# Optimization experiments

Hardware: AMD Instinct MI355X
Metric: run time of the kernel (lower is better)

Reference implementation:

```python
import jax, jax.numpy as jnp
import numpy as np
import math

HIDDEN = 2048
NUM_HEADS = 16
HEAD_DIM = HIDDEN // NUM_HEADS  # 128
B, T = 2, 2048
MAX_POS = 4096
ROPE_BASE = 10000.0


def _rope_cache(dim, max_pos, base):
    inv_freq = 1.0 / (base ** (jnp.arange(0, dim, 2, dtype=jnp.float32) / dim))
    t = jnp.arange(max_pos, dtype=jnp.float32)
    freqs = jnp.einsum('i,j->ij', t, inv_freq)        # [max_pos, dim/2]
    emb = jnp.concatenate([freqs, freqs], axis=-1)     # [max_pos, dim]
    return jnp.cos(emb), jnp.sin(emb)


def setup_inputs() -> dict:
    key = jax.random.key(0)
    ks = jax.random.split(key, 5)
    hidden_states = jax.random.normal(ks[0], (B, T, HIDDEN), dtype=jnp.float32)
    # additive causal mask, large negative (not -inf) for numerical safety
    causal = jnp.triu(jnp.full((T, T), -1e9, dtype=jnp.float32), k=1)
    attention_mask = causal[None, None, :, :]          # [1,1,T,T]
    position_ids = jnp.arange(T, dtype=jnp.int64)
    s = 1.0 / math.sqrt(HIDDEN)
    Wq = jax.random.normal(ks[1], (HIDDEN, HIDDEN), dtype=jnp.float32) * s
    Wk = jax.random.normal(ks[2], (HIDDEN, HIDDEN), dtype=jnp.float32) * s
    Wv = jax.random.normal(ks[3], (HIDDEN, HIDDEN), dtype=jnp.float32) * s
    Wo = jax.random.normal(ks[4], (HIDDEN, HIDDEN), dtype=jnp.float32) * s
    cos_cached, sin_cached = _rope_cache(HEAD_DIM, MAX_POS, ROPE_BASE)
    return {
        'hidden_states': hidden_states,
        'attention_mask': attention_mask,
        'position_ids': position_ids,
        'Wq': Wq, 'Wk': Wk, 'Wv': Wv, 'Wo': Wo,
        'cos_cached': cos_cached, 'sin_cached': sin_cached,
    }


def _apply_rope(x, cos, sin):
    # x: [B, T, nh, hd]; cos/sin: [T, 1, hd] (broadcast over heads)
    x1 = x[..., 0::2]
    x2 = x[..., 1::2]
    x_rot = jnp.stack([-x2, x1], axis=-1).reshape(x.shape)  # interleaved rotate
    return x * cos + x_rot * sin


def reference(hidden_states, attention_mask, position_ids, Wq, Wk, Wv, Wo,
              cos_cached, sin_cached):
    Bs, Ts, H = hidden_states.shape
    nh, hd = NUM_HEADS, HEAD_DIM
    q = (hidden_states @ Wq.T).reshape(Bs, Ts, nh, hd)
    k = (hidden_states @ Wk.T).reshape(Bs, Ts, nh, hd)
    v = (hidden_states @ Wv.T).reshape(Bs, Ts, nh, hd)
    cos = cos_cached[position_ids][:, None, :]  # [T,1,hd]
    sin = sin_cached[position_ids][:, None, :]
    q = _apply_rope(q, cos, sin)
    k = _apply_rope(k, cos, sin)
    # [B, nh, T, hd]
    q = q.transpose(0, 2, 1, 3)
    k = k.transpose(0, 2, 1, 3)
    v = v.transpose(0, 2, 1, 3)
    scores = jnp.einsum('bhqd,bhkd->bhqk', q, k) / math.sqrt(hd)
    scores = scores + attention_mask
    attn = jax.nn.softmax(scores, axis=-1)
    out = jnp.einsum('bhqk,bhkd->bhqd', attn, v)
    out = out.transpose(0, 2, 1, 3).reshape(Bs, Ts, H)
    return out @ Wo.T
```

## Files before the change

kernel.cpp:

```cpp
#include <hip/hip_runtime.h>
#include <cstdint>


typedef __bf16 v8bf __attribute__((ext_vector_type(8)));
typedef float  v4f  __attribute__((ext_vector_type(4)));
typedef float  f32x16 __attribute__((ext_vector_type(16)));

__device__ __forceinline__ uint16_t f2bf(float f) {
  union { float f; uint32_t u; } v; v.f = f;
  uint32_t u = v.u;
  return (uint16_t)((u + 0x7FFFu + ((u >> 16) & 1u)) >> 16);
}

__device__ __forceinline__ uint32_t cvtpk(float lo, float hi) {
  uint32_t w;
  asm("v_cvt_pk_bf16_f32 %0, %1, %2" : "=v"(w) : "v"(lo), "v"(hi));
  return w;
}

__device__ __forceinline__ void gload16(const void* g, void* l) {
  __builtin_amdgcn_global_load_lds(
      (const __attribute__((address_space(1))) void*)g,
      (__attribute__((address_space(3))) void*)l, 16, 0, 0);
}

__global__ void cvt_all_kernel(const float* __restrict__ s0, uint16_t* d0,
                               const float* __restrict__ s1, uint16_t* d1,
                               const float* __restrict__ s2, uint16_t* d2,
                               const float* __restrict__ s3, uint16_t* d3,
                               const float* __restrict__ s4, uint16_t* d4) {
  const float* src; uint16_t* dst; int n4;
  switch (blockIdx.y) {
    case 0: src = s0; dst = d0; n4 = 2097152; break;
    case 1: src = s1; dst = d1; n4 = 1048576; break;
    case 2: src = s2; dst = d2; n4 = 1048576; break;
    case 3: src = s3; dst = d3; n4 = 1048576; break;
    default: src = s4; dst = d4; n4 = 1048576; break;
  }
  int i = blockIdx.x * blockDim.x + threadIdx.x;
  int stride = gridDim.x * blockDim.x;
  for (; i < n4; i += stride) {
    float4 v = reinterpret_cast<const float4*>(src)[i];
    ushort4 o;
    o.x = f2bf(v.x); o.y = f2bf(v.y); o.z = f2bf(v.z); o.w = f2bf(v.w);
    reinterpret_cast<ushort4*>(dst)[i] = o;
  }
}

__device__ __forceinline__ void gemm128_mainloop(
    const uint16_t* __restrict__ A, const uint16_t* __restrict__ Bt,
    int m0, int n0, uint16_t* As, uint16_t* Bs, v4f acc[4][4]) {
  const int tid  = threadIdx.x;
  const int lane = tid & 63;
  const int w    = tid >> 6;
  const int wr   = w >> 1, wc = w & 1;
  const int lrow = lane & 15;
  const int lk8  = (lane >> 4) * 8;

  for (int k0 = 0; k0 < 2048; k0 += 64) {
#pragma unroll
    for (int i = 0; i < 4; ++i) {
      int chunk = i * 256 + tid;
      int row = chunk >> 3, seg = chunk & 7;
      gload16(A + (size_t)(m0 + row) * 2048 + k0 + seg * 8, As + chunk * 8);
    }
#pragma unroll
    for (int i = 0; i < 4; ++i) {
      int chunk = i * 256 + tid;
      int row = chunk >> 3, seg = chunk & 7;
      gload16(Bt + (size_t)(n0 + row) * 2048 + k0 + seg * 8, Bs + chunk * 8);
    }
    __syncthreads();
#pragma unroll
    for (int ks = 0; ks < 2; ++ks) {
      v8bf af[4], bfv[4];
#pragma unroll
      for (int mf = 0; mf < 4; ++mf)
        af[mf] = *reinterpret_cast<const v8bf*>(
            As + (wr * 64 + mf * 16 + lrow) * 64 + ks * 32 + lk8);
#pragma unroll
      for (int nf = 0; nf < 4; ++nf)
        bfv[nf] = *reinterpret_cast<const v8bf*>(
            Bs + (wc * 64 + nf * 16 + lrow) * 64 + ks * 32 + lk8);
#pragma unroll
      for (int mf = 0; mf < 4; ++mf)
#pragma unroll
        for (int nf = 0; nf < 4; ++nf)
          acc[mf][nf] = __builtin_amdgcn_mfma_f32_16x16x32_bf16(
              af[mf], bfv[nf], acc[mf][nf], 0, 0, 0);
    }
    __syncthreads();
  }
}

__global__ __launch_bounds__(256) void qkv_gemm_kernel(
    const uint16_t* __restrict__ Xbf,
    const uint16_t* __restrict__ Wqb, const uint16_t* __restrict__ Wkb,
    const uint16_t* __restrict__ Wvb,
    const float* __restrict__ cosc, const float* __restrict__ sinc,
    uint16_t* __restrict__ Qh, uint16_t* __restrict__ Kh,
    uint16_t* __restrict__ Vt) {
  __shared__ uint16_t As[128 * 64];
  __shared__ uint16_t Bs[128 * 64];
  const int id  = (blockIdx.z * 32 + blockIdx.y) * 16 + blockIdx.x;
  const int swz = (id & 7) * 192 + (id >> 3);
  const int which = swz >> 9;
  const int m0 = ((swz >> 4) & 31) * 128, n0 = (swz & 15) * 128;
  const uint16_t* Wb = (which == 0) ? Wqb : (which == 1) ? Wkb : Wvb;

  v4f acc[4][4];
#pragma unroll
  for (int i = 0; i < 4; ++i)
#pragma unroll
    for (int j = 0; j < 4; ++j) acc[i][j] = (v4f)0.0f;

  gemm128_mainloop(Xbf, Wb, m0, n0, As, Bs, acc);

  const int lane = threadIdx.x & 63;
  const int w = threadIdx.x >> 6, wr = w >> 1, wc = w & 1;
  const int lrow = lane & 15, lhi = lane >> 4;
  const int b = m0 >> 11;

  if (which < 2) {
    uint16_t* dst = (which == 0) ? Qh : Kh;
#pragma unroll
    for (int mf = 0; mf < 4; ++mf) {
#pragma unroll
      for (int nf = 0; nf < 4; ++nf) {
        const int n = n0 + wc * 64 + nf * 16 + lrow;
        const int head = n >> 7, d = n & 127;
#pragma unroll
        for (int r = 0; r < 4; ++r) {
          const int m = m0 + wr * 64 + mf * 16 + lhi * 4 + r;
          const int t = m & 2047;
          float v = acc[mf][nf][r];
          float p = __shfl_xor(v, 1);
          float rot = (n & 1) ? p : -p;
          float cf = cosc[t * 128 + d], sf = sinc[t * 128 + d];
          dst[((size_t)(b * 16 + head) * 2048 + t) * 128 + d] =
              f2bf(v * cf + rot * sf);
        }
      }
    }
  } else {
#pragma unroll
    for (int mf = 0; mf < 4; ++mf) {
#pragma unroll
      for (int nf = 0; nf < 4; ++nf) {
        const int n = n0 + wc * 64 + nf * 16 + lrow;
        const int head = n >> 7, d = n & 127;
        const int m = m0 + wr * 64 + mf * 16 + lhi * 4;
        const int t = m & 2047;
        ushort4 o;
        o.x = f2bf(acc[mf][nf][0]); o.y = f2bf(acc[mf][nf][1]);
        o.z = f2bf(acc[mf][nf][2]); o.w = f2bf(acc[mf][nf][3]);
        *reinterpret_cast<ushort4*>(
            &Vt[((size_t)(b * 16 + head) * 128 + d) * 2048 + t]) = o;
      }
    }
  }
}

__global__ __launch_bounds__(256, 2) void attn_kernel(
    const uint16_t* __restrict__ Qh, const uint16_t* __restrict__ Kh,
    const uint16_t* __restrict__ Vt, uint16_t* __restrict__ Ob) {
  __shared__ uint16_t Ks[2 * 64 * 128];
  __shared__ uint16_t Vs[2 * 128 * 64];

  const int id = blockIdx.x;
  const int qt = (id < 256) ? (15 - (id >> 5)) : ((id - 256) >> 5);
  const int bh = id & 31;
  const int tid = threadIdx.x, lane = tid & 63, w = tid >> 6;
  const int l31 = lane & 31, hi = lane >> 5;
  const size_t base = (size_t)bh * 2048 * 128;
  const int q0 = qt * 128 + w * 32;
  const int qr = q0 + l31;

  v8bf qf[8];
#pragma unroll
  for (int ks = 0; ks < 8; ++ks)
    qf[ks] = *reinterpret_cast<const v8bf*>(
        Qh + base + (size_t)qr * 128 + ks * 16 + hi * 8);

  f32x16 acc[4];
#pragma unroll
  for (int d = 0; d < 4; ++d) acc[d] = (f32x16)0.0f;
  float m = -1e30f, l = 0.0f;

  auto stage = [&](int buf, int kt) {
    uint16_t* Kd = Ks + buf * 8192;
    uint16_t* Vd = Vs + buf * 8192;
#pragma unroll
    for (int i = 0; i < 4; ++i) {
      int c = i * 256 + tid;
      int row = c >> 4, seg = c & 15;
      int sseg = seg ^ (row & 7);
      gload16(Kh + base + (size_t)(kt * 64 + row) * 128 + sseg * 8,
              Kd + c * 8);
    }
#pragma unroll
    for (int i = 0; i < 4; ++i) {
      int c = i * 256 + tid;
      int row = c >> 3, seg = c & 7;
      int sseg = seg ^ (row & 7);
      gload16(Vt + base + (size_t)row * 2048 + kt * 64 + sseg * 8,
              Vd + c * 8);
    }
  };

  const float sc = 0.08838834764831845f;
  const int nkt = 2 * (qt + 1);
  stage(0, 0);
  for (int kt = 0; kt < nkt; ++kt) {
    const int cur = kt & 1;
    __syncthreads();
    if (kt + 1 < nkt) stage(cur ^ 1, kt + 1);
    const uint16_t* Kc = Ks + cur * 8192;
    const uint16_t* Vc = Vs + cur * 8192;

    if (kt * 64 <= q0 + 31) {
      f32x16 s[2];
      s[0] = (f32x16)0.0f; s[1] = (f32x16)0.0f;
#pragma unroll
      for (int kb = 0; kb < 2; ++kb) {
        const int row = kb * 32 + l31;
        const int swz = row & 7;
#pragma unroll
        for (int ks = 0; ks < 8; ++ks) {
          const int seg = (ks * 2 + hi) ^ swz;
          v8bf kf = *reinterpret_cast<const v8bf*>(Kc + row * 128 + seg * 8);
          s[kb] = __builtin_amdgcn_mfma_f32_32x32x16_bf16(kf, qf[ks], s[kb],
                                                          0, 0, 0);
        }
      }
      if (kt * 64 + 63 > q0) {
#pragma unroll
        for (int kb = 0; kb < 2; ++kb)
#pragma unroll
          for (int q = 0; q < 4; ++q)
#pragma unroll
            for (int r = 0; r < 4; ++r) {
              const int kc = kt * 64 + kb * 32 + q * 8 + hi * 4 + r;
              float v = s[kb][q * 4 + r] * sc;
              s[kb][q * 4 + r] = (kc > qr) ? -1e30f : v;
            }
      } else {
#pragma unroll
        for (int kb = 0; kb < 2; ++kb)
#pragma unroll
          for (int g = 0; g < 16; ++g) s[kb][g] *= sc;
      }
      float t8[8];
#pragma unroll
      for (int g = 0; g < 8; ++g)
        t8[g] = fmaxf(fmaxf(s[0][g], s[0][g + 8]),
                      fmaxf(s[1][g], s[1][g + 8]));
      float mx = fmaxf(fmaxf(fmaxf(t8[0], t8[1]), fmaxf(t8[2], t8[3])),
                       fmaxf(fmaxf(t8[4], t8[5]), fmaxf(t8[6], t8[7])));
      mx = fmaxf(mx, __shfl_xor(mx, 32));
      if (!__all(mx - m <= 8.0f)) {
        const float mnew = fmaxf(m, mx);
        const float so = __expf(m - mnew);
        m = mnew;
        l *= so;
#pragma unroll
        for (int d = 0; d < 4; ++d)
#pragma unroll
          for (int g = 0; g < 16; ++g) acc[d][g] *= so;
      }
      float rs = 0.0f;
#pragma unroll
      for (int kb = 0; kb < 2; ++kb)
#pragma unroll
        for (int g = 0; g < 16; ++g) {
          const float pv = __expf(s[kb][g] - m);
          s[kb][g] = pv;
          rs += pv;
        }
      rs += __shfl_xor(rs, 32);
      l += rs;
      union BW { uint32_t w[4]; v8bf v; };
      BW pb[4];
#pragma unroll
      for (int kb = 0; kb < 2; ++kb)
#pragma unroll
        for (int sl = 0; sl < 2; ++sl) {
          uint32_t a0 = cvtpk(s[kb][8 * sl + 0], s[kb][8 * sl + 1]);
          uint32_t a1 = cvtpk(s[kb][8 * sl + 2], s[kb][8 * sl + 3]);
          uint32_t b0 = cvtpk(s[kb][8 * sl + 4], s[kb][8 * sl + 5]);
          uint32_t b1 = cvtpk(s[kb][8 * sl + 6], s[kb][8 * sl + 7]);
          asm("v_permlane32_swap_b32 %0, %1" : "+v"(a0), "+v"(b0));
          asm("v_permlane32_swap_b32 %0, %1" : "+v"(a1), "+v"(b1));
          BW& f = pb[kb * 2 + sl];
          f.w[0] = a0; f.w[1] = a1; f.w[2] = b0; f.w[3] = b1;
        }
#pragma unroll
      for (int d = 0; d < 4; ++d) {
        const int row = d * 32 + l31;
        const int swz = row & 7;
#pragma unroll
        for (int sl4 = 0; sl4 < 4; ++sl4) {
          const int seg = (sl4 * 2 + hi) ^ swz;
          v8bf va = *reinterpret_cast<const v8bf*>(Vc + row * 64 + seg * 8);
          acc[d] = __builtin_amdgcn_mfma_f32_32x32x16_bf16(va, pb[sl4].v,
                                                           acc[d], 0, 0, 0);
        }
      }
    }
  }

  const int b = bh >> 4, head = bh & 15;
  const float inv = 1.0f / l;
#pragma unroll
  for (int d = 0; d < 4; ++d)
#pragma unroll
    for (int q = 0; q < 4; ++q)
#pragma unroll
      for (int rp = 0; rp < 2; ++rp) {
        const int dd = d * 32 + q * 8 + hi * 4 + rp * 2;
        const uint32_t lo16 = f2bf(acc[d][q * 4 + rp * 2] * inv);
        const uint32_t hi16 = f2bf(acc[d][q * 4 + rp * 2 + 1] * inv);
        *reinterpret_cast<uint32_t*>(
            &Ob[((size_t)(b * 2048 + qr)) * 2048 + head * 128 + dd]) =
            lo16 | (hi16 << 16);
      }
}

__global__ __launch_bounds__(256) void out_gemm_kernel(
    const uint16_t* __restrict__ Abf, const uint16_t* __restrict__ Wob,
    float* __restrict__ out) {
  __shared__ uint16_t As[128 * 64];
  __shared__ uint16_t Bs[128 * 64];
  const int id  = blockIdx.y * 16 + blockIdx.x;
  const int swz = (id & 7) * 64 + (id >> 3);
  const int m0 = (swz >> 4) * 128, n0 = (swz & 15) * 128;
  v4f acc[4][4];
#pragma unroll
  for (int i = 0; i < 4; ++i)
#pragma unroll
    for (int j = 0; j < 4; ++j) acc[i][j] = (v4f)0.0f;

  gemm128_mainloop(Abf, Wob, m0, n0, As, Bs, acc);

  const int lane = threadIdx.x & 63;
  const int w = threadIdx.x >> 6, wr = w >> 1, wc = w & 1;
  const int lrow = lane & 15, lhi = lane >> 4;
#pragma unroll
  for (int mf = 0; mf < 4; ++mf)
#pragma unroll
    for (int nf = 0; nf < 4; ++nf) {
      const int n = n0 + wc * 64 + nf * 16 + lrow;
#pragma unroll
      for (int r = 0; r < 4; ++r) {
        const int m = m0 + wr * 64 + mf * 16 + lhi * 4 + r;
        out[(size_t)m * 2048 + n] = acc[mf][nf][r];
      }
    }
}

extern "C" void kernel_launch(void* const* d_in, const int* in_sizes, int n_in,
                              void* d_out, int out_size, void* d_ws,
                              size_t ws_size, hipStream_t stream) {
  const float* hidden = (const float*)d_in[0];
  const float* Wq = (const float*)d_in[3];
  const float* Wk = (const float*)d_in[4];
  const float* Wv = (const float*)d_in[5];
  const float* Wo = (const float*)d_in[6];
  const float* cosc = (const float*)d_in[7];
  const float* sinc = (const float*)d_in[8];
  float* out = (float*)d_out;

  uint16_t* Wqb = (uint16_t*)d_ws;
  uint16_t* Wkb = Wqb + 4194304;
  uint16_t* Wvb = Wkb + 4194304;
  uint16_t* Wvb2 = Wvb;
  uint16_t* Wob = Wvb + 4194304;
  uint16_t* Xbf = Wob + 4194304;
  uint16_t* Qh  = Xbf + 8388608;
  uint16_t* Kh  = Qh + 8388608;
  uint16_t* Vt  = Kh + 8388608;
  uint16_t* Ob  = Xbf;
  (void)Wvb2;

  cvt_all_kernel<<<dim3(512, 5), 256, 0, stream>>>(
      hidden, Xbf, Wq, Wqb, Wk, Wkb, Wv, Wvb, Wo, Wob);

  qkv_gemm_kernel<<<dim3(16, 32, 3), 256, 0, stream>>>(
      Xbf, Wqb, Wkb, Wvb, cosc, sinc, Qh, Kh, Vt);

  attn_kernel<<<dim3(512), 256, 0, stream>>>(Qh, Kh, Vt, Ob);

  out_gemm_kernel<<<dim3(16, 32), 256, 0, stream>>>(Ob, Wob, out);
}
```

Before: 435.8 us.

## Double-buffer GEMM LDS tiles with XOR swizzle to overlap loads and MFMA

Rewrites the shared GEMM mainloop so the global-to-LDS load of the next K tile is issued into a second buffer while the current tile is consumed, with one barrier per iteration instead of two. LDS reads use an XOR swizzle of the 16-byte segment by row to avoid bank conflicts. Both GEMM kernels get doubled LDS (64KB) and launch_bounds with a minimum of 2 blocks, which trades LDS capacity and register budget for the overlap.

```diff
diff --git a/kernel.cpp b/kernel.cpp
--- a/kernel.cpp
+++ b/kernel.cpp
@@ -55,33 +55,48 @@
   const int w    = tid >> 6;
   const int wr   = w >> 1, wc = w & 1;
   const int lrow = lane & 15;
-  const int lk8  = (lane >> 4) * 8;
-
-  for (int k0 = 0; k0 < 2048; k0 += 64) {
+  const int lhi  = lane >> 4;
+
+  auto stage = [&](int buf, int k0) {
+    uint16_t* Ad = As + buf * 8192;
+    uint16_t* Bd = Bs + buf * 8192;
 #pragma unroll
     for (int i = 0; i < 4; ++i) {
-      int chunk = i * 256 + tid;
-      int row = chunk >> 3, seg = chunk & 7;
-      gload16(A + (size_t)(m0 + row) * 2048 + k0 + seg * 8, As + chunk * 8);
+      int c = i * 256 + tid;
+      int row = c >> 3, seg = c & 7;
+      int sseg = seg ^ (row & 7);
+      gload16(A + (size_t)(m0 + row) * 2048 + k0 + sseg * 8, Ad + c * 8);
     }
 #pragma unroll
     for (int i = 0; i < 4; ++i) {
-      int chunk = i * 256 + tid;
-      int row = chunk >> 3, seg = chunk & 7;
-      gload16(Bt + (size_t)(n0 + row) * 2048 + k0 + seg * 8, Bs + chunk * 8);
-    }
+      int c = i * 256 + tid;
+      int row = c >> 3, seg = c & 7;
+      int sseg = seg ^ (row & 7);
+      gload16(Bt + (size_t)(n0 + row) * 2048 + k0 + sseg * 8, Bd + c * 8);
+    }
+  };
+
+  stage(0, 0);
+  for (int t = 0; t < 32; ++t) {
     __syncthreads();
+    if (t + 1 < 32) stage((t + 1) & 1, (t + 1) * 64);
+    const uint16_t* Ac = As + (t & 1) * 8192;
+    const uint16_t* Bc = Bs + (t & 1) * 8192;
 #pragma unroll
     for (int ks = 0; ks < 2; ++ks) {
       v8bf af[4], bfv[4];
 #pragma unroll
-      for (int mf = 0; mf < 4; ++mf)
-        af[mf] = *reinterpret_cast<const v8bf*>(
-            As + (wr * 64 + mf * 16 + lrow) * 64 + ks * 32 + lk8);
-#pragma unroll
-      for (int nf = 0; nf < 4; ++nf)
-        bfv[nf] = *reinterpret_cast<const v8bf*>(
-            Bs + (wc * 64 + nf * 16 + lrow) * 64 + ks * 32 + lk8);
+      for (int mf = 0; mf < 4; ++mf) {
+        const int ar = wr * 64 + mf * 16 + lrow;
+        const int seg = (ks * 4 + lhi) ^ (ar & 7);
+        af[mf] = *reinterpret_cast<const v8bf*>(Ac + ar * 64 + seg * 8);
+      }
+#pragma unroll
+      for (int nf = 0; nf < 4; ++nf) {
+        const int br = wc * 64 + nf * 16 + lrow;
+        const int seg = (ks * 4 + lhi) ^ (br & 7);
+        bfv[nf] = *reinterpret_cast<const v8bf*>(Bc + br * 64 + seg * 8);
+      }
 #pragma unroll
       for (int mf = 0; mf < 4; ++mf)
 #pragma unroll
@@ -89,19 +104,18 @@
           acc[mf][nf] = __builtin_amdgcn_mfma_f32_16x16x32_bf16(
               af[mf], bfv[nf], acc[mf][nf], 0, 0, 0);
     }
-    __syncthreads();
   }
 }
 
-__global__ __launch_bounds__(256) void qkv_gemm_kernel(
+__global__ __launch_bounds__(256, 2) void qkv_gemm_kernel(
     const uint16_t* __restrict__ Xbf,
     const uint16_t* __restrict__ Wqb, const uint16_t* __restrict__ Wkb,
     const uint16_t* __restrict__ Wvb,
     const float* __restrict__ cosc, const float* __restrict__ sinc,
     uint16_t* __restrict__ Qh, uint16_t* __restrict__ Kh,
     uint16_t* __restrict__ Vt) {
-  __shared__ uint16_t As[128 * 64];
-  __shared__ uint16_t Bs[128 * 64];
+  __shared__ uint16_t As[2 * 128 * 64];
+  __shared__ uint16_t Bs[2 * 128 * 64];
   const int id  = (blockIdx.z * 32 + blockIdx.y) * 16 + blockIdx.x;
   const int swz = (id & 7) * 192 + (id >> 3);
   const int which = swz >> 9;
@@ -326,11 +340,11 @@
       }
 }
 
-__global__ __launch_bounds__(256) void out_gemm_kernel(
+__global__ __launch_bounds__(256, 2) void out_gemm_kernel(
     const uint16_t* __restrict__ Abf, const uint16_t* __restrict__ Wob,
     float* __restrict__ out) {
-  __shared__ uint16_t As[128 * 64];
-  __shared__ uint16_t Bs[128 * 64];
+  __shared__ uint16_t As[2 * 128 * 64];
+  __shared__ uint16_t Bs[2 * 128 * 64];
   const int id  = blockIdx.y * 16 + blockIdx.x;
   const int swz = (id & 7) * 64 + (id >> 3);
   const int m0 = (swz >> 4) * 128, n0 = (swz & 15) * 128;
@@ -373,14 +387,12 @@
   uint16_t* Wqb = (uint16_t*)d_ws;
   uint16_t* Wkb = Wqb + 4194304;
   uint16_t* Wvb = Wkb + 4194304;
-  uint16_t* Wvb2 = Wvb;
   uint16_t* Wob = Wvb + 4194304;
   uint16_t* Xbf = Wob + 4194304;
   uint16_t* Qh  = Xbf + 8388608;
   uint16_t* Kh  = Qh + 8388608;
   uint16_t* Vt  = Kh + 8388608;
   uint16_t* Ob  = Xbf;
-  (void)Wvb2;
 
   cvt_all_kernel<<<dim3(512, 5), 256, 0, stream>>>(
       hidden, Xbf, Wq, Wqb, Wk, Wkb, Wv, Wvb, Wo, Wob);
```

Result: faster. 408.9 us (-6.2%).
